# Kernel tuning notes

Hardware: AMD Instinct MI355X
Metric: run time of the kernel (lower is better)

## Reference

```python
import jax, jax.numpy as jnp
import numpy as np

B, L_TOT, C = 64, 8192, 4
WIN = 16
H = 64
NL = 8
GROUPS = 8          # head groups
SA_GROUP = 4        # SortAttn group (hard-coded default)
GH = H * 2 // SA_GROUP   # 32
SEG = 4
CLS = 4
IN_SIZE = C * WIN   # 64 == H (all layers share input dim)


def _shuffle(x):
    # torch Shuffle: transpose(-1,-2).contiguous().view(original_shape)
    return jnp.swapaxes(x, -1, -2).reshape(x.shape)


def setup_inputs() -> dict:
    key = jax.random.key(0)
    ks = jax.random.split(key, 32)
    s = 0.1
    f32 = jnp.float32
    return {
        "x": jax.random.normal(ks[0], (B, L_TOT, C), f32),
        "h0_param": jnp.zeros((NL, 1, H), f32),
        "gru_w_ih": (jax.random.normal(ks[1], (NL, 3 * H, IN_SIZE), f32) * s),
        "gru_w_hh": (jax.random.normal(ks[2], (NL, 3 * H, H), f32) * s),
        "gru_b_ih": (jax.random.normal(ks[3], (NL, 3 * H), f32) * s),
        "gru_b_hh": (jax.random.normal(ks[4], (NL, 3 * H), f32) * s),
        "attn_w1": (jax.random.normal(ks[5], (NL, H, H), f32) * s),
        "attn_w2": (jax.random.normal(ks[6], (NL, GH, GH), f32) * s),
        "attn_w3": (jax.random.normal(ks[7], (NL, GH, GH), f32) * s),
        "attn_w4": (jax.random.normal(ks[8], (NL, H, 2 * H), f32) * s),
        "seg_w1": (jax.random.normal(ks[9], (SEG, H // GROUPS), f32) * s),
        "seg_b1": (jax.random.normal(ks[10], (SEG,), f32) * s),
        "seg_w2": (jax.random.normal(ks[11], (SEG, SEG), f32) * s),
        "seg_b2": (jax.random.normal(ks[12], (SEG,), f32) * s),
        "seg_w3": (jax.random.normal(ks[13], (SEG, SEG), f32) * s),
        "seg_b3": (jax.random.normal(ks[14], (SEG,), f32) * s),
        "seg_w4": (jax.random.normal(ks[15], (WIN, GROUPS), f32) * s),
        "seg_b4": (jax.random.normal(ks[16], (WIN,), f32) * s),
        "cls_w1": (jax.random.normal(ks[17], (CLS, H // GROUPS), f32) * s),
        "cls_b1": (jax.random.normal(ks[18], (CLS,), f32) * s),
        "cls_w2": (jax.random.normal(ks[19], (CLS, CLS), f32) * s),
        "cls_b2": (jax.random.normal(ks[20], (CLS,), f32) * s),
        "cls_w3": (jax.random.normal(ks[21], (CLS, CLS), f32) * s),
        "cls_b3": (jax.random.normal(ks[22], (CLS,), f32) * s),
        "cls_w4": (jax.random.normal(ks[23], (CLS, CLS * GROUPS), f32) * s),
        "cls_b4": (jax.random.normal(ks[24], (CLS,), f32) * s),
    }


def reference(x, h0_param, gru_w_ih, gru_w_hh, gru_b_ih, gru_b_hh,
              attn_w1, attn_w2, attn_w3, attn_w4,
              seg_w1, seg_b1, seg_w2, seg_b2, seg_w3, seg_b3, seg_w4, seg_b4,
              cls_w1, cls_b1, cls_w2, cls_b2, cls_w3, cls_b3, cls_w4, cls_b4):
    b, l, c = x.shape
    lw = l // WIN
    xs = x.reshape(b, lw, WIN * c)                     # (b, lw, IN_SIZE)
    h0 = jnp.broadcast_to(h0_param, (NL, b, H))        # hidden_0 * ones(1,b,1)

    def gru_cell(inp, h, w_ih, w_hh, b_ih, b_hh):
        gi = inp @ w_ih.T + b_ih                       # (b, 3H)
        gh = h @ w_hh.T + b_hh
        i_r, i_z, i_n = jnp.split(gi, 3, axis=1)
        h_r, h_z, h_n = jnp.split(gh, 3, axis=1)
        r = jax.nn.sigmoid(i_r + h_r)
        z = jax.nn.sigmoid(i_z + h_z)
        n = jnp.tanh(i_n + r * h_n)
        return (1.0 - z) * n + z * h

    def sort_attn(h, w1, w2, w3, w4):
        se = jnp.stack([h, jnp.sort(h, axis=1)], axis=1)   # (b, 2, H)
        a = se @ w1.T                                       # (b, 2, H)
        a = a.reshape(b, SA_GROUP, GH)                      # Flatten+Unflatten
        a = _shuffle(a) @ w2.T
        a = jax.nn.relu(_shuffle(a) @ w3.T)
        scores = jax.nn.sigmoid(a.reshape(b, SA_GROUP * GH) @ w4.T)  # (b, H)
        return h * scores

    def step(hidden, xt):
        inp = xt
        new = []
        for i in range(NL):
            hi = gru_cell(inp, hidden[i], gru_w_ih[i], gru_w_hh[i], gru_b_ih[i], gru_b_hh[i])
            hi = sort_attn(hi, attn_w1[i], attn_w2[i], attn_w3[i], attn_w4[i])
            new.append(hi)
            inp = hi
        return jnp.stack(new, axis=0), inp

    h_final, outs = jax.lax.scan(step, h0, jnp.swapaxes(xs, 0, 1))
    ys = jnp.swapaxes(outs, 0, 1)                      # (b, lw, H)

    # ---- seg head ----
    t = ys.reshape(b, lw, GROUPS, H // GROUPS)         # (b, lw, 8, 8)
    t = t @ seg_w1.T + seg_b1                          # (b, lw, 8, 4)
    t = _shuffle(t) @ seg_w2.T + seg_b2
    t = _shuffle(t) @ seg_w3.T + seg_b3
    t = t.reshape(b, lw, SEG, GROUPS)                  # Flatten(2)+Unflatten
    t = t @ seg_w4.T + seg_b4
    seg = jnp.swapaxes(t, -1, -2).reshape(b, lw * WIN, SEG)  # (b, l, 4)

    # ---- avg_pool1d(k=11, s=1) with 10 zero history frames ----
    pool_in = jnp.concatenate([jnp.zeros((b, 10, SEG), seg.dtype), seg], axis=1)
    cs = jnp.concatenate([jnp.zeros((b, 1, SEG), seg.dtype),
                          jnp.cumsum(pool_in, axis=1)], axis=1)
    pool_seg = (cs[:, 11:] - cs[:, :-11]) / 11.0       # (b, l, 4)

    # ---- cls head ----
    u = ys.reshape(b * lw, GROUPS, H // GROUPS)
    u = u @ cls_w1.T + cls_b1
    u = _shuffle(u) @ cls_w2.T + cls_b2
    u = jax.nn.relu(_shuffle(u) @ cls_w3.T + cls_b3)
    cls = u.reshape(b * lw, CLS * GROUPS) @ cls_w4.T + cls_b4
    cls = cls.reshape(b, lw, CLS).mean(axis=1)         # (b, 4)

    return (pool_seg, cls, ys, h_final, seg)
```

## Files before the change

kernel.cpp:

```cpp
#include <hip/hip_runtime.h>
#include <math.h>

#define LW  512

typedef unsigned short u16;
typedef float f32x4 __attribute__((ext_vector_type(4)));
typedef u16 u16x4 __attribute__((ext_vector_type(4)));
typedef u16 u16x8 __attribute__((ext_vector_type(8)));
typedef unsigned u32x2v __attribute__((ext_vector_type(2)));
typedef __bf16 bf16x8 __attribute__((ext_vector_type(8)));

__device__ __forceinline__ u16 f2bf(float f) {
    unsigned u = __builtin_bit_cast(unsigned, f);
    unsigned r = (u + 0x7fffu + ((u >> 16) & 1u)) >> 16;
    return (u16)r;
}
__device__ __forceinline__ float bf2f(u16 h) {
    unsigned u = ((unsigned)h) << 16;
    return __builtin_bit_cast(float, u);
}
__device__ __forceinline__ float sigm(float x) {
    return __builtin_amdgcn_rcpf(1.0f + __expf(-x));
}
__device__ __forceinline__ float tanhfast(float x) {
    return 1.0f - 2.0f * __builtin_amdgcn_rcpf(1.0f + __expf(2.0f * x));
}
__device__ __forceinline__ f32x4 mfma16(u16x8 a, u16x8 b, f32x4 c) {
    return __builtin_amdgcn_mfma_f32_16x16x32_bf16(
        __builtin_bit_cast(bf16x8, a), __builtin_bit_cast(bf16x8, b), c, 0, 0, 0);
}
__device__ __forceinline__ u16x8 ld8_8al(const u16* p) {
    u16x4 lo = *(const u16x4*)p;
    u16x4 hi = *(const u16x4*)(p + 4);
    return __builtin_shufflevector(lo, hi, 0, 1, 2, 3, 4, 5, 6, 7);
}
__device__ __forceinline__ unsigned ld_sys(const unsigned* p) {
    return __hip_atomic_load(p, __ATOMIC_RELAXED, __HIP_MEMORY_SCOPE_SYSTEM);
}
__device__ __forceinline__ void st_sys(unsigned* p, unsigned v) {
    __hip_atomic_store(p, v, __ATOMIC_RELAXED, __HIP_MEMORY_SCOPE_SYSTEM);
}
__device__ __forceinline__ void poll_ge(const unsigned* p, unsigned want) {
    while (ld_sys(p) < want) __builtin_amdgcn_s_sleep(2);
    asm volatile("" ::: "memory");
    __builtin_amdgcn_sched_barrier(0);
}
__device__ __forceinline__ void bar_lgkm() {
    asm volatile("s_waitcnt lgkmcnt(0)" ::: "memory");
    __builtin_amdgcn_s_barrier();
}

__global__ __launch_bounds__(256) void init_flags(unsigned* f) {
    f[blockIdx.x * 256 + threadIdx.x] = 0u;
}

__global__ __launch_bounds__(256, 1) void rnn_kernel(
    const float* __restrict__ x, const float* __restrict__ h0,
    const float* __restrict__ w_ih, const float* __restrict__ w_hh,
    const float* __restrict__ bih, const float* __restrict__ bhh,
    const float* __restrict__ aw1, const float* __restrict__ aw2,
    const float* __restrict__ aw3, const float* __restrict__ aw4,
    float* __restrict__ ys, float* __restrict__ hfin,
    unsigned* __restrict__ flags, unsigned* __restrict__ ring32, int D)
{
    const int l   = blockIdx.x >> 3;
    const int g   = blockIdx.x & 7;
    const int bb0 = g * 8;
    const int tid = threadIdx.x;
    const int w   = tid >> 6;
    const int ln  = tid & 63;
    const int l15 = ln & 15;
    const int l4  = ln >> 4;
    const bool bp = (D < LW);

    unsigned* mycnt  = flags + (size_t)(l * 8 + g) * 32;
    unsigned* pcnt   = flags + (size_t)((l - 1) * 8 + g) * 32;
    unsigned* myccnt = flags + 4096 + (size_t)(l * 8 + g) * 32;
    unsigned* nccnt  = flags + 4096 + (size_t)((l + 1) * 8 + g) * 32;

    __shared__ __align__(16) u16 Hin[2][16][72];
    __shared__ __align__(16) u16 hbf[16][72];
    __shared__ __align__(16) u16 se [16][72];
    __shared__ __align__(16) u16 a23[32][36];
    __shared__ __align__(16) u16 w4A[16][136];

    for (int i = tid; i < 16 * 72; i += 256) {
        int r = i / 72, c = i % 72;
        if (r >= 8) { Hin[0][r][c] = 0; Hin[1][r][c] = 0; hbf[r][c] = 0; }
    }
    for (int i = tid; i < 16 * 136; i += 256) {
        int r = i / 136;
        if (r >= 8) w4A[r][i % 136] = 0;
    }

    const int o = 16 * w + l15;
    auto ldw8 = [](const float* p) {
        float4 v0 = *(const float4*)p;
        float4 v1 = *(const float4*)(p + 4);
        u16x8 r;
        r[0] = f2bf(v0.x); r[1] = f2bf(v0.y); r[2] = f2bf(v0.z); r[3] = f2bf(v0.w);
        r[4] = f2bf(v1.x); r[5] = f2bf(v1.y); r[6] = f2bf(v1.z); r[7] = f2bf(v1.w);
        return r;
    };
    const float* ih = w_ih + l * 12288;
    const float* hh = w_hh + l * 12288;
    u16x8 Br[4], Bz[4], Bni[2], Bnh[2], B1f[2], B2f[2], B3f[2], B4f[4];
    Br[0] = ldw8(ih + o * 64 + l4 * 8);        Br[1] = ldw8(ih + o * 64 + 32 + l4 * 8);
    Br[2] = ldw8(hh + o * 64 + l4 * 8);        Br[3] = ldw8(hh + o * 64 + 32 + l4 * 8);
    Bz[0] = ldw8(ih + (64 + o) * 64 + l4 * 8); Bz[1] = ldw8(ih + (64 + o) * 64 + 32 + l4 * 8);
    Bz[2] = ldw8(hh + (64 + o) * 64 + l4 * 8); Bz[3] = ldw8(hh + (64 + o) * 64 + 32 + l4 * 8);
    Bni[0] = ldw8(ih + (128 + o) * 64 + l4 * 8); Bni[1] = ldw8(ih + (128 + o) * 64 + 32 + l4 * 8);
    Bnh[0] = ldw8(hh + (128 + o) * 64 + l4 * 8); Bnh[1] = ldw8(hh + (128 + o) * 64 + 32 + l4 * 8);
    B1f[0] = ldw8(aw1 + l * 4096 + o * 64 + l4 * 8);
    B1f[1] = ldw8(aw1 + l * 4096 + o * 64 + 32 + l4 * 8);
    B2f[0] = ldw8(aw2 + l * 1024 + l15 * 32 + l4 * 8);
    B2f[1] = ldw8(aw2 + l * 1024 + (16 + l15) * 32 + l4 * 8);
    B3f[0] = ldw8(aw3 + l * 1024 + l15 * 32 + l4 * 8);
    B3f[1] = ldw8(aw3 + l * 1024 + (16 + l15) * 32 + l4 * 8);
    #pragma unroll
    for (int kk = 0; kk < 4; ++kk)
        B4f[kk] = ldw8(aw4 + l * 8192 + o * 128 + kk * 32 + l4 * 8);

    const float brs  = bih[l * 192 + o]       + bhh[l * 192 + o];
    const float bzs  = bih[l * 192 + 64 + o]  + bhh[l * 192 + 64 + o];
    const float bnis = bih[l * 192 + 128 + o];
    const float bnhs = bhh[l * 192 + 128 + o];

    float hreg[4];
    {
        float hv = h0[l * 64 + o];
        #pragma unroll
        for (int j = 0; j < 4; ++j) hreg[j] = hv;
        if (l4 < 2) {
            u16 hb = f2bf(hv);
            #pragma unroll
            for (int j = 0; j < 4; ++j) hbf[l4 * 4 + j][o] = hb;
        }
    }

    float4 stf = {0.f, 0.f, 0.f, 0.f};
    unsigned st0 = 0, st1 = 0;
    if (w >= 2) {
        const int rr = (tid - 128) >> 4, c4 = ((tid - 128) & 15) * 4;
        if (l == 0) {
            float4 a = *(const float4*)(x + (size_t)(bb0 + rr) * 32768 + c4);
            u16x4 hv;
            hv[0] = f2bf(a.x); hv[1] = f2bf(a.y); hv[2] = f2bf(a.z); hv[3] = f2bf(a.w);
            *(u16x4*)&Hin[0][rr][c4] = hv;
            stf = *(const float4*)(x + (size_t)(bb0 + rr) * 32768 + 64 + c4);
        } else {
            poll_ge(pcnt, 1u);
            const unsigned* sp0 = ring32 + ((size_t)((l - 1) * 8 + g) * D + 0) * 256 + rr * 32 + (c4 >> 1);
            unsigned a0 = ld_sys(sp0), a1 = ld_sys(sp0 + 1);
            u32x2v dv = {a0, a1};
            *(u16x4*)&Hin[0][rr][c4] = __builtin_bit_cast(u16x4, dv);
            poll_ge(pcnt, 2u);
            const unsigned* sp1 = ring32 + ((size_t)((l - 1) * 8 + g) * D + 1) * 256 + rr * 32 + (c4 >> 1);
            st0 = ld_sys(sp1); st1 = ld_sys(sp1 + 1);
        }
    }
    __syncthreads();

    for (int t = 0; t < LW; ++t) {
        float hg[4];
        {
            u16x8 Ag0 = *(const u16x8*)&Hin[t & 1][l15][l4 * 8];
            u16x8 Ag1 = *(const u16x8*)&Hin[t & 1][l15][32 + l4 * 8];
            u16x8 Ah0 = *(const u16x8*)&hbf[l15][l4 * 8];
            u16x8 Ah1 = *(const u16x8*)&hbf[l15][32 + l4 * 8];
            f32x4 z4 = {0.f, 0.f, 0.f, 0.f};
            f32x4 aR = z4, aZ = z4, aNI = z4, aNH = z4;
            aR = mfma16(Ag0, Br[0], aR);  aR = mfma16(Ag1, Br[1], aR);
            aR = mfma16(Ah0, Br[2], aR);  aR = mfma16(Ah1, Br[3], aR);
            aZ = mfma16(Ag0, Bz[0], aZ);  aZ = mfma16(Ag1, Bz[1], aZ);
            aZ = mfma16(Ah0, Bz[2], aZ);  aZ = mfma16(Ah1, Bz[3], aZ);
            aNI = mfma16(Ag0, Bni[0], aNI); aNI = mfma16(Ag1, Bni[1], aNI);
            aNH = mfma16(Ah0, Bnh[0], aNH); aNH = mfma16(Ah1, Bnh[1], aNH);
            #pragma unroll
            for (int j = 0; j < 4; ++j) {
                float r  = sigm(aR[j] + brs);
                float zz = sigm(aZ[j] + bzs);
                float nn = tanhfast(aNI[j] + bnis + r * (aNH[j] + bnhs));
                hg[j] = (1.0f - zz) * nn + zz * hreg[j];
            }
            if (l4 < 2) {
                #pragma unroll
                for (int j = 0; j < 4; ++j) se[l4 * 4 + j][o] = f2bf(hg[j]);
            }
        }
        bar_lgkm();

        {
            float v0 = bf2f(se[2 * w][ln]);
            float v1 = bf2f(se[2 * w + 1][ln]);
            #pragma unroll
            for (int kk = 2; kk <= 64; kk <<= 1) {
                #pragma unroll
                for (int j = kk >> 1; j > 0; j >>= 1) {
                    float o0 = __shfl_xor(v0, j);
                    float o1 = __shfl_xor(v1, j);
                    bool keepmin = (((ln & kk) == 0) == ((ln & j) == 0));
                    v0 = keepmin ? fminf(v0, o0) : fmaxf(v0, o0);
                    v1 = keepmin ? fminf(v1, o1) : fmaxf(v1, o1);
                }
            }
            se[8 + 2 * w][ln] = f2bf(v0);
            se[9 + 2 * w][ln] = f2bf(v1);
        }
        bar_lgkm();

        {
            u16x8 As0 = *(const u16x8*)&se[l15][l4 * 8];
            u16x8 As1 = *(const u16x8*)&se[l15][32 + l4 * 8];
            f32x4 c = {0.f, 0.f, 0.f, 0.f};
            c = mfma16(As0, B1f[0], c);
            c = mfma16(As1, B1f[1], c);
            #pragma unroll
            for (int j = 0; j < 4; ++j) {
                int m = l4 * 4 + j;
                int p = m >> 3, b = m & 7;
                int f = p * 64 + o;
                int q = (f & 31) * 4 + (f >> 5);
                a23[b * 4 + (q >> 5)][q & 31] = f2bf(c[j]);
            }
        }
        bar_lgkm();

        if (w < 2) {
            const int Rb0 = 16 * w;
            u16x8 a2a = ld8_8al(&a23[Rb0 + l15][l4 * 8]);
            f32x4 z4 = {0.f, 0.f, 0.f, 0.f};
            f32x4 c2[2];
            c2[0] = mfma16(a2a, B2f[0], z4);
            c2[1] = mfma16(a2a, B2f[1], z4);
            #pragma unroll
            for (int nt = 0; nt < 2; ++nt)
                #pragma unroll
                for (int j = 0; j < 4; ++j) {
                    int m = Rb0 + l4 * 4 + j;
                    int b = m >> 2, i2 = m & 3;
                    int n = 16 * nt + l15;
                    int f2 = i2 * 32 + n;
                    int q2 = (f2 & 31) * 4 + (f2 >> 5);
                    a23[b * 4 + (q2 >> 5)][q2 & 31] = f2bf(c2[nt][j]);
                }
            asm volatile("s_waitcnt lgkmcnt(0)" ::: "memory");
            __builtin_amdgcn_sched_barrier(0);
            u16x8 a3a = ld8_8al(&a23[Rb0 + l15][l4 * 8]);
            f32x4 c3[2];
            c3[0] = mfma16(a3a, B3f[0], z4);
            c3[1] = mfma16(a3a, B3f[1], z4);
            #pragma unroll
            for (int nt = 0; nt < 2; ++nt)
                #pragma unroll
                for (int j = 0; j < 4; ++j) {
                    int m = Rb0 + l4 * 4 + j;
                    int b = m >> 2, i3 = m & 3;
                    int n = 16 * nt + l15;
                    w4A[b][i3 * 32 + n] = f2bf(fmaxf(c3[nt][j], 0.0f));
                }
        } else {
            const int rr = (tid - 128) >> 4, c4 = ((tid - 128) & 15) * 4;
            if (t + 1 < LW) {
                u16x4 hv;
                if (l == 0) {
                    hv[0] = f2bf(stf.x); hv[1] = f2bf(stf.y);
                    hv[2] = f2bf(stf.z); hv[3] = f2bf(stf.w);
                } else {
                    u32x2v dv = {st0, st1};
                    hv = __builtin_bit_cast(u16x4, dv);
                }
                *(u16x4*)&Hin[(t + 1) & 1][rr][c4] = hv;
            }
            if (t + 2 < LW) {
                if (l == 0) {
                    stf = *(const float4*)(x + (size_t)(bb0 + rr) * 32768 + (t + 2) * 64 + c4);
                } else {
                    poll_ge(pcnt, (unsigned)(t + 3));
                    const unsigned* sp = ring32
                        + ((size_t)((l - 1) * 8 + g) * D + ((t + 2) & (D - 1))) * 256
                        + rr * 32 + (c4 >> 1);
                    st0 = ld_sys(sp); st1 = ld_sys(sp + 1);
                }
            }
        }
        bar_lgkm();
        if (bp && l > 0 && tid == 0)
            st_sys(myccnt, (unsigned)(t + 2));

        {
            u16x8 A40 = *(const u16x8*)&w4A[l15][l4 * 8];
            u16x8 A41 = *(const u16x8*)&w4A[l15][32 + l4 * 8];
            u16x8 A42 = *(const u16x8*)&w4A[l15][64 + l4 * 8];
            u16x8 A43 = *(const u16x8*)&w4A[l15][96 + l4 * 8];
            f32x4 cs = {0.f, 0.f, 0.f, 0.f};
            cs = mfma16(A40, B4f[0], cs);
            cs = mfma16(A41, B4f[1], cs);
            cs = mfma16(A42, B4f[2], cs);
            cs = mfma16(A43, B4f[3], cs);

            float hn[4]; u16 hb[4];
            #pragma unroll
            for (int j = 0; j < 4; ++j) {
                hn[j] = hg[j] * sigm(cs[j]);
                hreg[j] = hn[j];
                hb[j] = f2bf(hn[j]);
            }
            if (l4 < 2) {
                #pragma unroll
                for (int j = 0; j < 4; ++j) {
                    int row = l4 * 4 + j;
                    hbf[row][o] = hb[j];
                    if (l == 7) ys[(((size_t)(bb0 + row) << 9) + t) * 64 + o] = hn[j];
                    if (t == 511) hfin[((l << 6) + bb0 + row) * 64 + o] = hn[j];
                }
            }
            if (l < 7) {
                if (bp && t >= D)
                    poll_ge(nccnt, (unsigned)(t - D + 1));
                unsigned* slotp = ring32 + ((size_t)(l * 8 + g) * D + (t & (D - 1))) * 256;
                #pragma unroll
                for (int j = 0; j < 4; ++j) {
                    unsigned ob = (unsigned)__shfl_xor((int)(unsigned)hb[j], 1) & 0xffffu;
                    if (l4 < 2 && !(l15 & 1)) {
                        unsigned word = (unsigned)hb[j] | (ob << 16);
                        st_sys(&slotp[(l4 * 4 + j) * 32 + (o >> 1)], word);
                    }
                }
            }
        }
        if (l < 7) asm volatile("s_waitcnt vmcnt(0) lgkmcnt(0)" ::: "memory");
        else       asm volatile("s_waitcnt lgkmcnt(0)" ::: "memory");
        __builtin_amdgcn_s_barrier();
        if (l < 7 && tid == 0)
            st_sys(mycnt, (unsigned)(t + 1));
    }
}

__global__ __launch_bounds__(256) void heads_kernel(
    const float* __restrict__ ys,
    const float* __restrict__ sw1, const float* __restrict__ sb1,
    const float* __restrict__ sw2, const float* __restrict__ sb2,
    const float* __restrict__ sw3, const float* __restrict__ sb3,
    const float* __restrict__ sw4, const float* __restrict__ sb4,
    const float* __restrict__ cw1, const float* __restrict__ cb1,
    const float* __restrict__ cw2, const float* __restrict__ cb2,
    const float* __restrict__ cw3, const float* __restrict__ cb3,
    const float* __restrict__ cw4, const float* __restrict__ cb4,
    float* __restrict__ seg_out, float* __restrict__ cls_tmp)
{
    const int idx = blockIdx.x * 256 + threadIdx.x;
    if (idx >= 64 * LW) return;
    const int b = idx >> 9, t = idx & 511;

    float y[64];
    const float4* yp = (const float4*)(ys + (size_t)idx * 64);
    #pragma unroll
    for (int i = 0; i < 16; ++i) {
        float4 v = yp[i];
        y[4 * i + 0] = v.x; y[4 * i + 1] = v.y; y[4 * i + 2] = v.z; y[4 * i + 3] = v.w;
    }

    float t1[8][4], t2[8][4], t3[8][4];

    #pragma unroll
    for (int g = 0; g < 8; ++g)
        #pragma unroll
        for (int s = 0; s < 4; ++s) {
            float acc = sb1[s];
            #pragma unroll
            for (int k = 0; k < 8; ++k) acc = fmaf(y[g * 8 + k], sw1[s * 8 + k], acc);
            t1[g][s] = acc;
        }
    #pragma unroll
    for (int i = 0; i < 8; ++i) {
        float sh[4];
        #pragma unroll
        for (int j = 0; j < 4; ++j) { int m = i * 4 + j; sh[j] = t1[m & 7][m >> 3]; }
        #pragma unroll
        for (int s = 0; s < 4; ++s) {
            float acc = sb2[s];
            #pragma unroll
            for (int j = 0; j < 4; ++j) acc = fmaf(sh[j], sw2[s * 4 + j], acc);
            t2[i][s] = acc;
        }
    }
    #pragma unroll
    for (int i = 0; i < 8; ++i) {
        float sh[4];
        #pragma unroll
        for (int j = 0; j < 4; ++j) { int m = i * 4 + j; sh[j] = t2[m & 7][m >> 3]; }
        #pragma unroll
        for (int s = 0; s < 4; ++s) {
            float acc = sb3[s];
            #pragma unroll
            for (int j = 0; j < 4; ++j) acc = fmaf(sh[j], sw3[s * 4 + j], acc);
            t3[i][s] = acc;
        }
    }
    #pragma unroll
    for (int w = 0; w < 16; ++w) {
        float o4[4];
        #pragma unroll
        for (int s = 0; s < 4; ++s) {
            float acc = sb4[w];
            #pragma unroll
            for (int j = 0; j < 8; ++j) {
                int f = s * 8 + j;
                acc = fmaf(t3[f >> 2][f & 3], sw4[w * 8 + j], acc);
            }
            o4[s] = acc;
        }
        float4 vv = {o4[0], o4[1], o4[2], o4[3]};
        ((float4*)seg_out)[b * 8192 + t * 16 + w] = vv;
    }

    #pragma unroll
    for (int g = 0; g < 8; ++g)
        #pragma unroll
        for (int s = 0; s < 4; ++s) {
            float acc = cb1[s];
            #pragma unroll
            for (int k = 0; k < 8; ++k) acc = fmaf(y[g * 8 + k], cw1[s * 8 + k], acc);
            t1[g][s] = acc;
        }
    #pragma unroll
    for (int i = 0; i < 8; ++i) {
        float sh[4];
        #pragma unroll
        for (int j = 0; j < 4; ++j) { int m = i * 4 + j; sh[j] = t1[m & 7][m >> 3]; }
        #pragma unroll
        for (int s = 0; s < 4; ++s) {
            float acc = cb2[s];
            #pragma unroll
            for (int j = 0; j < 4; ++j) acc = fmaf(sh[j], cw2[s * 4 + j], acc);
            t2[i][s] = acc;
        }
    }
    #pragma unroll
    for (int i = 0; i < 8; ++i) {
        float sh[4];
        #pragma unroll
        for (int j = 0; j < 4; ++j) { int m = i * 4 + j; sh[j] = t2[m & 7][m >> 3]; }
        #pragma unroll
        for (int s = 0; s < 4; ++s) {
            float acc = cb3[s];
            #pragma unroll
            for (int j = 0; j < 4; ++j) acc = fmaf(sh[j], cw3[s * 4 + j], acc);
            t3[i][s] = fmaxf(acc, 0.f);
        }
    }
    float cc[4];
    #pragma unroll
    for (int c = 0; c < 4; ++c) {
        float acc = cb4[c];
        #pragma unroll
        for (int k = 0; k < 32; ++k)
            acc = fmaf(t3[k >> 2][k & 3], cw4[c * 32 + k], acc);
        cc[c] = acc;
    }
    float4 cv = {cc[0], cc[1], cc[2], cc[3]};
    ((float4*)cls_tmp)[idx] = cv;
}

__global__ __launch_bounds__(256) void cls_reduce_kernel(
    const float* __restrict__ cls_tmp, float* __restrict__ cls_out)
{
    const int tid = threadIdx.x;
    const int b = tid >> 2, q = tid & 3;
    float ax = 0.f, ay = 0.f, az = 0.f, aw = 0.f;
    for (int t = q; t < 512; t += 4) {
        float4 v = ((const float4*)cls_tmp)[b * 512 + t];
        ax += v.x; ay += v.y; az += v.z; aw += v.w;
    }
    ax += __shfl_xor(ax, 1); ay += __shfl_xor(ay, 1);
    az += __shfl_xor(az, 1); aw += __shfl_xor(aw, 1);
    ax += __shfl_xor(ax, 2); ay += __shfl_xor(ay, 2);
    az += __shfl_xor(az, 2); aw += __shfl_xor(aw, 2);
    if (q == 0) {
        float4 rv = {ax / 512.f, ay / 512.f, az / 512.f, aw / 512.f};
        ((float4*)cls_out)[b] = rv;
    }
}

__global__ __launch_bounds__(256) void pool_kernel(
    const float* __restrict__ seg, float* __restrict__ pool_out)
{
    const int idx = blockIdx.x * 256 + threadIdx.x;
    if (idx >= 64 * 8192) return;
    const int b = idx >> 13, ll = idx & 8191;
    float ax = 0.f, ay = 0.f, az = 0.f, aw = 0.f;
    int j0 = ll - 10; if (j0 < 0) j0 = 0;
    for (int j = j0; j <= ll; ++j) {
        float4 v = ((const float4*)seg)[b * 8192 + j];
        ax += v.x; ay += v.y; az += v.z; aw += v.w;
    }
    const float inv = 1.0f / 11.0f;
    float4 ov = {ax * inv, ay * inv, az * inv, aw * inv};
    ((float4*)pool_out)[idx] = ov;
}

extern "C" void kernel_launch(void* const* d_in, const int* in_sizes, int n_in,
                              void* d_out, int out_size, void* d_ws, size_t ws_size,
                              hipStream_t stream)
{
    const float* x    = (const float*)d_in[0];
    const float* h0   = (const float*)d_in[1];
    const float* w_ih = (const float*)d_in[2];
    const float* w_hh = (const float*)d_in[3];
    const float* bihp = (const float*)d_in[4];
    const float* bhhp = (const float*)d_in[5];
    const float* aw1  = (const float*)d_in[6];
    const float* aw2  = (const float*)d_in[7];
    const float* aw3  = (const float*)d_in[8];
    const float* aw4  = (const float*)d_in[9];
    const float* sw1  = (const float*)d_in[10];
    const float* sb1  = (const float*)d_in[11];
    const float* sw2  = (const float*)d_in[12];
    const float* sb2  = (const float*)d_in[13];
    const float* sw3  = (const float*)d_in[14];
    const float* sb3  = (const float*)d_in[15];
    const float* sw4  = (const float*)d_in[16];
    const float* sb4  = (const float*)d_in[17];
    const float* cw1  = (const float*)d_in[18];
    const float* cb1  = (const float*)d_in[19];
    const float* cw2  = (const float*)d_in[20];
    const float* cb2  = (const float*)d_in[21];
    const float* cw3  = (const float*)d_in[22];
    const float* cb3  = (const float*)d_in[23];
    const float* cw4  = (const float*)d_in[24];
    const float* cb4  = (const float*)d_in[25];

    float* out      = (float*)d_out;
    float* pool_out = out;
    float* cls_out  = out + 2097152;
    float* ys_out   = out + 2097408;
    float* hfin     = out + 4194560;
    float* seg_out  = out + 4227328;
    float* cls_tmp  = pool_out;

    unsigned* flags  = (unsigned*)d_ws;
    unsigned* ring32 = (unsigned*)((char*)d_ws + 32768);

    size_t slots = (ws_size > 32768) ? (ws_size - 32768) / (56ull * 256 * 4) : 8;
    int D = 512;
    if (slots < 512) {
        D = 8;
        while ((size_t)(D * 2) <= slots && D < 512) D <<= 1;
    }

    init_flags<<<32, 256, 0, stream>>>(flags);
    rnn_kernel<<<64, 256, 0, stream>>>(x, h0, w_ih, w_hh, bihp, bhhp,
                                       aw1, aw2, aw3, aw4, ys_out, hfin,
                                       flags, ring32, D);
    heads_kernel<<<128, 256, 0, stream>>>(ys_out, sw1, sb1, sw2, sb2, sw3, sb3, sw4, sb4,
                                          cw1, cb1, cw2, cb2, cw3, cb3, cw4, cb4,
                                          seg_out, cls_tmp);
    cls_reduce_kernel<<<1, 256, 0, stream>>>(cls_tmp, cls_out);
    pool_kernel<<<2048, 256, 0, stream>>>(seg_out, pool_out);
}
```

Before: 1.678 ms.

## Use per-wave progress flags and prefetch next-step input fragments

Each of the four waves now publishes its own progress flag after its ring stores drain, deferred into the following step. This replaces the single end-of-step vmcnt wait plus barrier plus one thread's flag store, and consumers poll all four flags and take the minimum. The GRU input A-fragments for the next step are read from LDS early, alongside the w4 MFMA, and the consumer-credit poll is moved ahead of the gating math. The aim is to take the global-store drain and the flag publication off the per-step critical path between layers. In exchange, producers signal one step later and consumers must poll four words instead of one.

Measured after the change: 1.537 ms. 8.4% less time.

```diff
diff --git a/kernel.cpp b/kernel.cpp
--- a/kernel.cpp
+++ b/kernel.cpp
@@ -42,6 +42,18 @@
 }
 __device__ __forceinline__ void poll_ge(const unsigned* p, unsigned want) {
     while (ld_sys(p) < want) __builtin_amdgcn_s_sleep(2);
+    asm volatile("" ::: "memory");
+    __builtin_amdgcn_sched_barrier(0);
+}
+__device__ __forceinline__ void poll4(const unsigned* p, unsigned want) {
+    for (;;) {
+        unsigned m0 = ld_sys(p + 0), m1 = ld_sys(p + 1);
+        unsigned m2 = ld_sys(p + 2), m3 = ld_sys(p + 3);
+        unsigned a = m0 < m1 ? m0 : m1;
+        unsigned b = m2 < m3 ? m2 : m3;
+        if ((a < b ? a : b) >= want) break;
+        __builtin_amdgcn_s_sleep(2);
+    }
     asm volatile("" ::: "memory");
     __builtin_amdgcn_sched_barrier(0);
 }
@@ -73,8 +85,8 @@
     const int l4  = ln >> 4;
     const bool bp = (D < LW);
 
-    unsigned* mycnt  = flags + (size_t)(l * 8 + g) * 32;
-    unsigned* pcnt   = flags + (size_t)((l - 1) * 8 + g) * 32;
+    unsigned* myflag = flags + (size_t)(l * 8 + g) * 32;
+    unsigned* pflag  = flags + (size_t)((l - 1) * 8 + g) * 32;
     unsigned* myccnt = flags + 4096 + (size_t)(l * 8 + g) * 32;
     unsigned* nccnt  = flags + 4096 + (size_t)((l + 1) * 8 + g) * 32;
 
@@ -149,33 +161,34 @@
             *(u16x4*)&Hin[0][rr][c4] = hv;
             stf = *(const float4*)(x + (size_t)(bb0 + rr) * 32768 + 64 + c4);
         } else {
-            poll_ge(pcnt, 1u);
+            poll4(pflag, 1u);
             const unsigned* sp0 = ring32 + ((size_t)((l - 1) * 8 + g) * D + 0) * 256 + rr * 32 + (c4 >> 1);
             unsigned a0 = ld_sys(sp0), a1 = ld_sys(sp0 + 1);
             u32x2v dv = {a0, a1};
             *(u16x4*)&Hin[0][rr][c4] = __builtin_bit_cast(u16x4, dv);
-            poll_ge(pcnt, 2u);
+            poll4(pflag, 2u);
             const unsigned* sp1 = ring32 + ((size_t)((l - 1) * 8 + g) * D + 1) * 256 + rr * 32 + (c4 >> 1);
             st0 = ld_sys(sp1); st1 = ld_sys(sp1 + 1);
         }
     }
     __syncthreads();
+
+    u16x8 pAg0 = *(const u16x8*)&Hin[0][l15][l4 * 8];
+    u16x8 pAg1 = *(const u16x8*)&Hin[0][l15][32 + l4 * 8];
 
     for (int t = 0; t < LW; ++t) {
         float hg[4];
         {
-            u16x8 Ag0 = *(const u16x8*)&Hin[t & 1][l15][l4 * 8];
-            u16x8 Ag1 = *(const u16x8*)&Hin[t & 1][l15][32 + l4 * 8];
             u16x8 Ah0 = *(const u16x8*)&hbf[l15][l4 * 8];
             u16x8 Ah1 = *(const u16x8*)&hbf[l15][32 + l4 * 8];
             f32x4 z4 = {0.f, 0.f, 0.f, 0.f};
             f32x4 aR = z4, aZ = z4, aNI = z4, aNH = z4;
-            aR = mfma16(Ag0, Br[0], aR);  aR = mfma16(Ag1, Br[1], aR);
-            aR = mfma16(Ah0, Br[2], aR);  aR = mfma16(Ah1, Br[3], aR);
-            aZ = mfma16(Ag0, Bz[0], aZ);  aZ = mfma16(Ag1, Bz[1], aZ);
-            aZ = mfma16(Ah0, Bz[2], aZ);  aZ = mfma16(Ah1, Bz[3], aZ);
-            aNI = mfma16(Ag0, Bni[0], aNI); aNI = mfma16(Ag1, Bni[1], aNI);
-            aNH = mfma16(Ah0, Bnh[0], aNH); aNH = mfma16(Ah1, Bnh[1], aNH);
+            aR = mfma16(pAg0, Br[0], aR);  aR = mfma16(pAg1, Br[1], aR);
+            aR = mfma16(Ah0, Br[2], aR);   aR = mfma16(Ah1, Br[3], aR);
+            aZ = mfma16(pAg0, Bz[0], aZ);  aZ = mfma16(pAg1, Bz[1], aZ);
+            aZ = mfma16(Ah0, Bz[2], aZ);   aZ = mfma16(Ah1, Bz[3], aZ);
+            aNI = mfma16(pAg0, Bni[0], aNI); aNI = mfma16(pAg1, Bni[1], aNI);
+            aNH = mfma16(Ah0, Bnh[0], aNH);  aNH = mfma16(Ah1, Bnh[1], aNH);
             #pragma unroll
             for (int j = 0; j < 4; ++j) {
                 float r  = sigm(aR[j] + brs);
@@ -209,6 +222,10 @@
         }
         bar_lgkm();
 
+        if (l < 7) {
+            asm volatile("s_waitcnt vmcnt(0)" ::: "memory");
+            if (ln == 0) st_sys(myflag + w, (unsigned)t);
+        }
         {
             u16x8 As0 = *(const u16x8*)&se[l15][l4 * 8];
             u16x8 As1 = *(const u16x8*)&se[l15][32 + l4 * 8];
@@ -276,7 +293,7 @@
                 if (l == 0) {
                     stf = *(const float4*)(x + (size_t)(bb0 + rr) * 32768 + (t + 2) * 64 + c4);
                 } else {
-                    poll_ge(pcnt, (unsigned)(t + 3));
+                    poll4(pflag, (unsigned)(t + 3));
                     const unsigned* sp = ring32
                         + ((size_t)((l - 1) * 8 + g) * D + ((t + 2) & (D - 1))) * 256
                         + rr * 32 + (c4 >> 1);
@@ -293,12 +310,18 @@
             u16x8 A41 = *(const u16x8*)&w4A[l15][32 + l4 * 8];
             u16x8 A42 = *(const u16x8*)&w4A[l15][64 + l4 * 8];
             u16x8 A43 = *(const u16x8*)&w4A[l15][96 + l4 * 8];
+            pAg0 = *(const u16x8*)&Hin[(t + 1) & 1][l15][l4 * 8];
+            pAg1 = *(const u16x8*)&Hin[(t + 1) & 1][l15][32 + l4 * 8];
             f32x4 cs = {0.f, 0.f, 0.f, 0.f};
             cs = mfma16(A40, B4f[0], cs);
             cs = mfma16(A41, B4f[1], cs);
             cs = mfma16(A42, B4f[2], cs);
             cs = mfma16(A43, B4f[3], cs);
 
+            if (bp && l < 7 && t >= D) {
+                poll_ge(nccnt, (unsigned)(t - D + 1));
+            }
+            unsigned* slotp = ring32 + ((size_t)(l * 8 + g) * D + (t & (D - 1))) * 256;
             float hn[4]; u16 hb[4];
             #pragma unroll
             for (int j = 0; j < 4; ++j) {
@@ -316,9 +339,6 @@
                 }
             }
             if (l < 7) {
-                if (bp && t >= D)
-                    poll_ge(nccnt, (unsigned)(t - D + 1));
-                unsigned* slotp = ring32 + ((size_t)(l * 8 + g) * D + (t & (D - 1))) * 256;
                 #pragma unroll
                 for (int j = 0; j < 4; ++j) {
                     unsigned ob = (unsigned)__shfl_xor((int)(unsigned)hb[j], 1) & 0xffffu;
@@ -329,11 +349,12 @@
                 }
             }
         }
-        if (l < 7) asm volatile("s_waitcnt vmcnt(0) lgkmcnt(0)" ::: "memory");
-        else       asm volatile("s_waitcnt lgkmcnt(0)" ::: "memory");
-        __builtin_amdgcn_s_barrier();
-        if (l < 7 && tid == 0)
-            st_sys(mycnt, (unsigned)(t + 1));
+        bar_lgkm();
+    }
+
+    if (l < 7) {
+        asm volatile("s_waitcnt vmcnt(0)" ::: "memory");
+        if (ln == 0) st_sys(myflag + w, 512u);
     }
 }
 
```
